# Kernel optimization log

Measured on AMD Instinct MI355X. Metric: run time of the kernel, lower is better.

## Reference

```python
import jax, jax.numpy as jnp
import numpy as np

K = 3          # deformable conv kernel size
DG = 4         # deformable groups
PAD = (K - 1) // 2


def _deform_conv(x, offset, w, dg=DG, pad=PAD):
    """DCNv1 forward (stride=1, dilation=1, conv groups=1, no bias).

    x:      [B, C, H, W]
    offset: [B, dg*K*K*2, H, W]  layout per group: (dy, dx) per kernel tap
    w:      [O, C, K, K]
    """
    B, C, H, W = x.shape
    O = w.shape[0]
    k2 = K * K
    gC = C // dg

    off = offset.reshape(B, dg, k2, 2, H, W)
    dy, dx = off[:, :, :, 0], off[:, :, :, 1]          # [B, dg, k2, H, W]

    ky, kx = jnp.meshgrid(jnp.arange(K), jnp.arange(K), indexing='ij')
    ky = ky.reshape(k2).astype(x.dtype)
    kx = kx.reshape(k2).astype(x.dtype)
    hi = jnp.arange(H, dtype=x.dtype)
    wi = jnp.arange(W, dtype=x.dtype)

    # absolute fractional sample coords: p0 - pad + kernel tap + learned offset
    ys = hi[None, None, None, :, None] - pad + ky[None, None, :, None, None] + dy
    xs = wi[None, None, None, None, :] - pad + kx[None, None, :, None, None] + dx

    y0 = jnp.floor(ys)
    x0 = jnp.floor(xs)
    ly = ys - y0   # bilinear weights
    lx = xs - x0
    y0 = y0.astype(jnp.int32)
    x0 = x0.astype(jnp.int32)

    xg = x.reshape(B, dg, gC, H * W)

    def gather(yi, xi):
        # zero padding outside the image (per-corner validity, matches mmcv)
        valid = ((yi >= 0) & (yi < H) & (xi >= 0) & (xi < W)).astype(x.dtype)
        idx = (jnp.clip(yi, 0, H - 1) * W + jnp.clip(xi, 0, W - 1)).reshape(B, dg, -1)
        vals = jax.vmap(jax.vmap(lambda t, i: t[:, i]))(xg, idx)  # [B,dg,gC,k2*H*W]
        return vals.reshape(B, dg, gC, k2, H, W) * valid[:, :, None]

    # bilinear interpolation of the 4 corners
    sampled = ((1 - ly) * (1 - lx))[:, :, None] * gather(y0,     x0) \
            + ((1 - ly) * lx      )[:, :, None] * gather(y0,     x0 + 1) \
            + (ly       * (1 - lx))[:, :, None] * gather(y0 + 1, x0) \
            + (ly       * lx      )[:, :, None] * gather(y0 + 1, x0 + 1)
    # sampled: [B, dg, gC, k2, H, W]

    wr = w.reshape(O, dg, gC, k2)
    return jnp.einsum('bgckhw,ogck->bohw', sampled, wr)


def setup_inputs() -> dict:
    key = jax.random.key(0)
    k0, k1, k2k, k3 = jax.random.split(key, 4)
    B, C, H, W, O = 2, 256, 128, 128, 256
    oc = DG * K * K * 2
    x = jax.random.normal(k0, (B, C, H, W), jnp.float32)
    # offset conv is zero-init in the module; use small random values so the
    # deformable sampling path is actually exercised
    w_offset = jax.random.normal(k1, (oc, C, 1, 1), jnp.float32) * 0.01
    b_offset = jax.random.normal(k2k, (oc,), jnp.float32) * 0.01
    w_deform = jax.random.normal(k3, (O, C, K, K), jnp.float32) / np.sqrt(C * K * K)
    return {"x": x, "w_offset": w_offset, "b_offset": b_offset, "w_deform": w_deform}


def reference(x, w_offset, b_offset, w_deform):
    # 1x1 conv predicting offsets
    offset = jnp.einsum('bchw,oc->bohw', x, w_offset[:, :, 0, 0]) \
             + b_offset[None, :, None, None]
    # deformable conv + ReLU
    return jax.nn.relu(_deform_conv(x, offset, w_deform))
```

## Files before the change

### kernel.cpp

```cpp
#include <hip/hip_runtime.h>

#define HW 16384

typedef __attribute__((ext_vector_type(4))) float f32x4;
typedef __attribute__((ext_vector_type(8))) short bf16x8;
typedef __attribute__((ext_vector_type(4))) int i32x4;

static __device__ __forceinline__ float bf2f(short s) {
    return __uint_as_float(((unsigned)(unsigned short)s) << 16);
}
static __device__ __forceinline__ unsigned short f2bf(float f) {
    unsigned u = __float_as_uint(f);
    unsigned r = u + 0x7fffu + ((u >> 16) & 1u);
    return (unsigned short)(r >> 16);
}
static __device__ __forceinline__ int cvt_pk_bf16(float lo, float hi) {
    int r;
    asm("v_cvt_pk_bf16_f32 %0, %1, %2" : "=v"(r) : "v"(lo), "v"(hi));
    return r;
}

__global__ __launch_bounds__(256) void prep_kernel(
    const float* __restrict__ x, const float* __restrict__ wd,
    const float* __restrict__ woff,
    unsigned short* __restrict__ xT, unsigned short* __restrict__ Wc2,
    unsigned short* __restrict__ Wo2)
{
    int bid = blockIdx.x;
    int tid = threadIdx.x;
    if (bid < 2048) {
        __shared__ float tl[64][65];
        int ct = bid & 3, pt = (bid >> 2) & 255, b = bid >> 10;
        int l = tid & 63, ci4 = tid >> 6;
        const float* xb = x + ((size_t)(b * 256 + ct * 64)) * HW + pt * 64;
        for (int ci = ci4; ci < 64; ci += 4)
            tl[ci][l] = xb[(size_t)ci * HW + l];
        __syncthreads();
        unsigned short* ob = xT + ((size_t)(b * HW + pt * 64)) * 256 + ct * 64;
        #pragma unroll
        for (int j2 = 0; j2 < 2; ++j2) {
            int slot = tid + j2 * 256;
            int p = slot >> 3, sl = slot & 7;
            i32x4 st;
            #pragma unroll
            for (int kq = 0; kq < 4; ++kq)
                ((int*)&st)[kq] = cvt_pk_bf16(tl[sl*8 + kq*2][p], tl[sl*8 + kq*2 + 1][p]);
            *(i32x4*)(ob + (size_t)p * 256 + sl * 8) = st;
        }
    } else if (bid < 2336) {
        int slot = (bid - 2048) * 256 + tid;
        int l  = slot & 63;
        int ks = (slot >> 6) & 1;
        int mi = (slot >> 7) & 3;
        int q  = (slot >> 9) & 3;
        int kc = slot >> 11;
        int g = kc / 9, tap = kc - g * 9;
        int o = q * 64 + mi * 16 + (l & 15);
        int cgb = (ks * 4 + (l >> 4)) * 8;
        unsigned short* dst = Wc2 + (size_t)slot * 8;
        const float* src = wd + (size_t)o * 2304 + tap;
        #pragma unroll
        for (int e = 0; e < 8; ++e)
            dst[e] = f2bf(src[(size_t)(g * 64 + cgb + e) * 9]);
    } else {
        int slot = (bid - 2336) * 256 + tid;
        int kk = slot / 320;
        int rem = slot - kk * 320;
        int o = rem >> 2, jq = rem & 3;
        unsigned short* dst = Wo2 + (size_t)slot * 8;
        #pragma unroll
        for (int e = 0; e < 8; ++e)
            dst[e] = (o < 72) ? f2bf(woff[(size_t)o * 256 + kk * 32 + jq * 8 + e]) : (unsigned short)0;
    }
}

__global__ __launch_bounds__(256, 3) void deform_kernel(
    const unsigned short* __restrict__ xT, const unsigned short* __restrict__ Wc2,
    const unsigned short* __restrict__ Wo2, const float* __restrict__ b_off,
    float* __restrict__ out)
{
    __shared__ int   c_yx[2304];
    __shared__ float c_ly[2304];
    __shared__ float c_lx[2304];
    __shared__ __align__(16) short Sl[4096];

    const int t    = threadIdx.x;
    const int lane = t & 63;
    const int q    = t >> 6;
    const int lr   = lane & 15, lq = lane >> 4;
    const int gp0  = blockIdx.x << 6;
    const int b    = gp0 >> 14;
    const int hw0  = gp0 & 16383;
    const int h    = hw0 >> 7;
    const int w0   = hw0 & 127;

    {
        bf16x8 xb[8];
        const unsigned short* xrow = xT + ((size_t)(b * HW + hw0 + q * 16 + lr)) * 256 + lq * 8;
        #pragma unroll
        for (int kk = 0; kk < 8; ++kk)
            xb[kk] = *(const bf16x8*)(xrow + kk * 32);
        #pragma unroll
        for (int mi = 0; mi < 5; ++mi) {
            f32x4 oa = (f32x4)0.f;
            #pragma unroll
            for (int kk = 0; kk < 8; ++kk) {
                bf16x8 af = *(const bf16x8*)(Wo2 + (size_t)((kk * 80 + mi * 16 + lr) * 32 + lq * 8));
                oa = __builtin_amdgcn_mfma_f32_16x16x32_bf16(af, xb[kk], oa, 0, 0, 0);
            }
            #pragma unroll
            for (int ri = 0; ri < 2; ++ri) {
                int gt = mi * 8 + lq * 2 + ri;
                if (gt < 36) {
                    int p = q * 16 + lr;
                    float dy = oa[ri * 2]     + b_off[2 * gt];
                    float dx = oa[ri * 2 + 1] + b_off[2 * gt + 1];
                    int tap = gt % 9;
                    float ys = (float)(h - 1 + tap / 3) + dy;
                    float xs = (float)(w0 + p - 1 + tap % 3) + dx;
                    float fy = floorf(ys), fx = floorf(xs);
                    int y0 = (int)fy, x0 = (int)fx;
                    c_yx[gt * 64 + p] = (y0 & 0xffff) | (x0 << 16);
                    c_ly[gt * 64 + p] = ys - fy;
                    c_lx[gt * 64 + p] = xs - fx;
                }
            }
        }
    }
    __syncthreads();

    f32x4 acc[4][4];
    #pragma unroll
    for (int mi = 0; mi < 4; ++mi)
        #pragma unroll
        for (int nj = 0; nj < 4; ++nj)
            acc[mi][nj] = (f32x4)0.f;

    const unsigned short* xbase = xT + ((size_t)b * HW) * 256;

    for (int g = 0; g < 4; ++g)
    for (int tap = 0; tap < 9; ++tap) {
        const int kc = g * 9 + tap;
        bf16x8 a_[4][2];
        {
            const unsigned short* wb = Wc2 + (size_t)(kc * 16 + q * 4) * 1024 + lane * 8;
            #pragma unroll
            for (int mi = 0; mi < 4; ++mi)
                #pragma unroll
                for (int ks = 0; ks < 2; ++ks)
                    a_[mi][ks] = *(const bf16x8*)(wb + mi * 1024 + ks * 512);
        }
        #pragma unroll
        for (int pg = 0; pg < 2; ++pg) {
            int p   = q * 16 + pg * 8 + (lane >> 3);
            int sl  = lane & 7;
            int idx = kc * 64 + p;
            int yx = c_yx[idx];
            int y0 = (int)(short)(yx & 0xffff);
            int x0 = yx >> 16;
            float ly = c_ly[idx], lx = c_lx[idx];
            float omy = 1.f - ly, omx = 1.f - lx;
            float vy0 = ((unsigned)y0       < 128u) ? 1.f : 0.f;
            float vy1 = ((unsigned)(y0 + 1) < 128u) ? 1.f : 0.f;
            float vx0 = ((unsigned)x0       < 128u) ? 1.f : 0.f;
            float vx1 = ((unsigned)(x0 + 1) < 128u) ? 1.f : 0.f;
            float w00 = omy * omx * vy0 * vx0, w01 = omy * lx * vy0 * vx1;
            float w10 = ly  * omx * vy1 * vx0, w11 = ly  * lx * vy1 * vx1;
            int y0c = min(max(y0, 0), 127), y1c = min(max(y0 + 1, 0), 127);
            int x0c = min(max(x0, 0), 127), x1c = min(max(x0 + 1, 0), 127);
            const unsigned short* cb = xbase + (size_t)(g * 64 + sl * 8);
            bf16x8 v00 = *(const bf16x8*)(cb + (size_t)(y0c * 128 + x0c) * 256);
            bf16x8 v01 = *(const bf16x8*)(cb + (size_t)(y0c * 128 + x1c) * 256);
            bf16x8 v10 = *(const bf16x8*)(cb + (size_t)(y1c * 128 + x0c) * 256);
            bf16x8 v11 = *(const bf16x8*)(cb + (size_t)(y1c * 128 + x1c) * 256);
            float sv[8];
            #pragma unroll
            for (int e = 0; e < 8; ++e)
                sv[e] = w00 * bf2f(v00[e]) + w01 * bf2f(v01[e])
                      + w10 * bf2f(v10[e]) + w11 * bf2f(v11[e]);
            i32x4 st;
            #pragma unroll
            for (int kq = 0; kq < 4; ++kq)
                ((int*)&st)[kq] = cvt_pk_bf16(sv[kq * 2], sv[kq * 2 + 1]);
            ((i32x4*)Sl)[p * 8 + (sl ^ (p & 7))] = st;
        }
        __syncthreads();
        #pragma unroll
        for (int ks = 0; ks < 2; ++ks) {
            bf16x8 bb[4];
            #pragma unroll
            for (int nj = 0; nj < 4; ++nj) {
                int pp = nj * 16 + lr;
                bb[nj] = *(const bf16x8*)&((const i32x4*)Sl)[pp * 8 + ((ks * 4 + lq) ^ (pp & 7))];
            }
            #pragma unroll
            for (int mi = 0; mi < 4; ++mi)
                #pragma unroll
                for (int nj = 0; nj < 4; ++nj)
                    acc[mi][nj] = __builtin_amdgcn_mfma_f32_16x16x32_bf16(
                        a_[mi][ks], bb[nj], acc[mi][nj], 0, 0, 0);
        }
        __syncthreads();
    }

    #pragma unroll
    for (int mi = 0; mi < 4; ++mi)
        #pragma unroll
        for (int nj = 0; nj < 4; ++nj)
            #pragma unroll
            for (int r = 0; r < 4; ++r) {
                int o  = q * 64 + mi * 16 + lq * 4 + r;
                int pp = nj * 16 + lr;
                out[((size_t)(b * 256 + o) << 14) + hw0 + pp] = fmaxf(acc[mi][nj][r], 0.f);
            }
}

extern "C" void kernel_launch(void* const* d_in, const int* in_sizes, int n_in,
                              void* d_out, int out_size, void* d_ws, size_t ws_size,
                              hipStream_t stream) {
    const float* x     = (const float*)d_in[0];
    const float* w_off = (const float*)d_in[1];
    const float* b_off = (const float*)d_in[2];
    const float* w_def = (const float*)d_in[3];
    float* out = (float*)d_out;

    unsigned short* xT  = (unsigned short*)d_ws;
    unsigned short* Wc2 = (unsigned short*)((char*)d_ws + 16777216);
    unsigned short* Wo2 = (unsigned short*)((char*)d_ws + 17956864);

    prep_kernel<<<2346, 256, 0, stream>>>(x, w_def, w_off, xT, Wc2, Wo2);
    deform_kernel<<<512, 256, 0, stream>>>(xT, Wc2, Wo2, b_off, out);
}
```

Baseline: 169.1 us.

## Double-buffer sampled tile, widen deform kernel to 512 threads, vectorize prep loads

The deform kernel now runs 512 threads per block, each wave owning 32 output channels instead of 64. Sampled-tile LDS buffers are double-buffered so the bilinear gather for the next tap overlaps the MFMA work on the current one, which drops one barrier per iteration. Block IDs are remapped across batches and rows, and the prep transpose uses float4 global loads. The cost is more LDS per block and more per-thread register pressure under the new launch bounds, which may reduce occupancy.

```diff
diff --git a/kernel.cpp b/kernel.cpp
--- a/kernel.cpp
+++ b/kernel.cpp
@@ -31,10 +31,17 @@
     if (bid < 2048) {
         __shared__ float tl[64][65];
         int ct = bid & 3, pt = (bid >> 2) & 255, b = bid >> 10;
-        int l = tid & 63, ci4 = tid >> 6;
         const float* xb = x + ((size_t)(b * 256 + ct * 64)) * HW + pt * 64;
-        for (int ci = ci4; ci < 64; ci += 4)
-            tl[ci][l] = xb[(size_t)ci * HW + l];
+        #pragma unroll
+        for (int j = 0; j < 4; ++j) {
+            int slot = tid + j * 256;
+            int c = slot >> 4, p4 = slot & 15;
+            float4 v = *(const float4*)(xb + (size_t)c * HW + p4 * 4);
+            tl[c][p4 * 4 + 0] = v.x;
+            tl[c][p4 * 4 + 1] = v.y;
+            tl[c][p4 * 4 + 2] = v.z;
+            tl[c][p4 * 4 + 3] = v.w;
+        }
         __syncthreads();
         unsigned short* ob = xT + ((size_t)(b * HW + pt * 64)) * 256 + ct * 64;
         #pragma unroll
@@ -52,10 +59,10 @@
         int l  = slot & 63;
         int ks = (slot >> 6) & 1;
         int mi = (slot >> 7) & 3;
-        int q  = (slot >> 9) & 3;
+        int q4 = (slot >> 9) & 3;
         int kc = slot >> 11;
         int g = kc / 9, tap = kc - g * 9;
-        int o = q * 64 + mi * 16 + (l & 15);
+        int o = q4 * 64 + mi * 16 + (l & 15);
         int cgb = (ks * 4 + (l >> 4)) * 8;
         unsigned short* dst = Wc2 + (size_t)slot * 8;
         const float* src = wd + (size_t)o * 2304 + tap;
@@ -74,7 +81,7 @@
     }
 }
 
-__global__ __launch_bounds__(256, 3) void deform_kernel(
+__global__ __launch_bounds__(512, 4) void deform_kernel(
     const unsigned short* __restrict__ xT, const unsigned short* __restrict__ Wc2,
     const unsigned short* __restrict__ Wo2, const float* __restrict__ b_off,
     float* __restrict__ out)
@@ -82,45 +89,49 @@
     __shared__ int   c_yx[2304];
     __shared__ float c_ly[2304];
     __shared__ float c_lx[2304];
-    __shared__ __align__(16) short Sl[4096];
+    __shared__ __align__(16) short Sbuf[2][4096];
 
     const int t    = threadIdx.x;
     const int lane = t & 63;
     const int q    = t >> 6;
     const int lr   = lane & 15, lq = lane >> 4;
-    const int gp0  = blockIdx.x << 6;
+    int bid = blockIdx.x;
+    bid = (bid & 7) * 64 + (bid >> 3);
+    const int gp0  = bid << 6;
     const int b    = gp0 >> 14;
     const int hw0  = gp0 & 16383;
     const int h    = hw0 >> 7;
     const int w0   = hw0 & 127;
 
     {
-        bf16x8 xb[8];
-        const unsigned short* xrow = xT + ((size_t)(b * HW + hw0 + q * 16 + lr)) * 256 + lq * 8;
+        const int p16 = (q & 3) * 16;
+        bf16x8 xv[8];
+        const unsigned short* xrow = xT + ((size_t)(b * HW + hw0 + p16 + lr)) * 256 + lq * 8;
         #pragma unroll
         for (int kk = 0; kk < 8; ++kk)
-            xb[kk] = *(const bf16x8*)(xrow + kk * 32);
-        #pragma unroll
-        for (int mi = 0; mi < 5; ++mi) {
+            xv[kk] = *(const bf16x8*)(xrow + kk * 32);
+        const int mi0 = (q < 4) ? 0 : 3;
+        const int nmi = (q < 4) ? 3 : 2;
+        for (int im = 0; im < nmi; ++im) {
+            int mi = mi0 + im;
             f32x4 oa = (f32x4)0.f;
             #pragma unroll
             for (int kk = 0; kk < 8; ++kk) {
                 bf16x8 af = *(const bf16x8*)(Wo2 + (size_t)((kk * 80 + mi * 16 + lr) * 32 + lq * 8));
-                oa = __builtin_amdgcn_mfma_f32_16x16x32_bf16(af, xb[kk], oa, 0, 0, 0);
+                oa = __builtin_amdgcn_mfma_f32_16x16x32_bf16(af, xv[kk], oa, 0, 0, 0);
             }
             #pragma unroll
             for (int ri = 0; ri < 2; ++ri) {
                 int gt = mi * 8 + lq * 2 + ri;
                 if (gt < 36) {
-                    int p = q * 16 + lr;
+                    int p = p16 + lr;
                     float dy = oa[ri * 2]     + b_off[2 * gt];
                     float dx = oa[ri * 2 + 1] + b_off[2 * gt + 1];
                     int tap = gt % 9;
                     float ys = (float)(h - 1 + tap / 3) + dy;
                     float xs = (float)(w0 + p - 1 + tap % 3) + dx;
                     float fy = floorf(ys), fx = floorf(xs);
-                    int y0 = (int)fy, x0 = (int)fx;
-                    c_yx[gt * 64 + p] = (y0 & 0xffff) | (x0 << 16);
+                    c_yx[gt * 64 + p] = ((int)fy & 0xffff) | ((int)fx << 16);
                     c_ly[gt * 64 + p] = ys - fy;
                     c_lx[gt * 64 + p] = xs - fx;
                 }
@@ -129,32 +140,63 @@
     }
     __syncthreads();
 
-    f32x4 acc[4][4];
+    f32x4 acc[2][4];
     #pragma unroll
-    for (int mi = 0; mi < 4; ++mi)
+    for (int mi = 0; mi < 2; ++mi)
         #pragma unroll
         for (int nj = 0; nj < 4; ++nj)
             acc[mi][nj] = (f32x4)0.f;
 
     const unsigned short* xbase = xT + ((size_t)b * HW) * 256;
-
-    for (int g = 0; g < 4; ++g)
-    for (int tap = 0; tap < 9; ++tap) {
-        const int kc = g * 9 + tap;
-        bf16x8 a_[4][2];
-        {
-            const unsigned short* wb = Wc2 + (size_t)(kc * 16 + q * 4) * 1024 + lane * 8;
-            #pragma unroll
-            for (int mi = 0; mi < 4; ++mi)
-                #pragma unroll
-                for (int ks = 0; ks < 2; ++ks)
-                    a_[mi][ks] = *(const bf16x8*)(wb + mi * 1024 + ks * 512);
-        }
-        #pragma unroll
-        for (int pg = 0; pg < 2; ++pg) {
-            int p   = q * 16 + pg * 8 + (lane >> 3);
-            int sl  = lane & 7;
-            int idx = kc * 64 + p;
+    const int ppix = q * 8 + (lane >> 3);
+    const int sl   = lane & 7;
+    const int q4   = q >> 1;
+    const int mo   = (q & 1) * 2;
+
+    {
+        int idx = ppix;
+        int yx = c_yx[idx];
+        int y0 = (int)(short)(yx & 0xffff);
+        int x0 = yx >> 16;
+        float ly = c_ly[idx], lx = c_lx[idx];
+        float omy = 1.f - ly, omx = 1.f - lx;
+        float vy0 = ((unsigned)y0       < 128u) ? 1.f : 0.f;
+        float vy1 = ((unsigned)(y0 + 1) < 128u) ? 1.f : 0.f;
+        float vx0 = ((unsigned)x0       < 128u) ? 1.f : 0.f;
+        float vx1 = ((unsigned)(x0 + 1) < 128u) ? 1.f : 0.f;
+        float w00 = omy * omx * vy0 * vx0, w01 = omy * lx * vy0 * vx1;
+        float w10 = ly  * omx * vy1 * vx0, w11 = ly  * lx * vy1 * vx1;
+        int y0c = min(max(y0, 0), 127), y1c = min(max(y0 + 1, 0), 127);
+        int x0c = min(max(x0, 0), 127), x1c = min(max(x0 + 1, 0), 127);
+        const unsigned short* cb = xbase + (size_t)(sl * 8);
+        bf16x8 v00 = *(const bf16x8*)(cb + (size_t)(y0c * 128 + x0c) * 256);
+        bf16x8 v01 = *(const bf16x8*)(cb + (size_t)(y0c * 128 + x1c) * 256);
+        bf16x8 v10 = *(const bf16x8*)(cb + (size_t)(y1c * 128 + x0c) * 256);
+        bf16x8 v11 = *(const bf16x8*)(cb + (size_t)(y1c * 128 + x1c) * 256);
+        float sv[8];
+        #pragma unroll
+        for (int e = 0; e < 8; ++e)
+            sv[e] = w00 * bf2f(v00[e]) + w01 * bf2f(v01[e])
+                  + w10 * bf2f(v10[e]) + w11 * bf2f(v11[e]);
+        i32x4 st;
+        #pragma unroll
+        for (int kq = 0; kq < 4; ++kq)
+            ((int*)&st)[kq] = cvt_pk_bf16(sv[kq * 2], sv[kq * 2 + 1]);
+        ((i32x4*)Sbuf[0])[ppix * 8 + (sl ^ (ppix & 7))] = st;
+    }
+    __syncthreads();
+
+    short* Sc = Sbuf[0];
+    short* Sn = Sbuf[1];
+
+    for (int kc = 0; kc < 36; ++kc) {
+        bf16x8 v00, v01, v10, v11;
+        float w00, w01, w10, w11;
+        const bool pf = (kc < 35);
+        if (pf) {
+            int kn = kc + 1;
+            int g  = kn / 9;
+            int idx = kn * 64 + ppix;
             int yx = c_yx[idx];
             int y0 = (int)(short)(yx & 0xffff);
             int x0 = yx >> 16;
@@ -164,15 +206,41 @@
             float vy1 = ((unsigned)(y0 + 1) < 128u) ? 1.f : 0.f;
             float vx0 = ((unsigned)x0       < 128u) ? 1.f : 0.f;
             float vx1 = ((unsigned)(x0 + 1) < 128u) ? 1.f : 0.f;
-            float w00 = omy * omx * vy0 * vx0, w01 = omy * lx * vy0 * vx1;
-            float w10 = ly  * omx * vy1 * vx0, w11 = ly  * lx * vy1 * vx1;
+            w00 = omy * omx * vy0 * vx0; w01 = omy * lx * vy0 * vx1;
+            w10 = ly  * omx * vy1 * vx0; w11 = ly  * lx * vy1 * vx1;
             int y0c = min(max(y0, 0), 127), y1c = min(max(y0 + 1, 0), 127);
             int x0c = min(max(x0, 0), 127), x1c = min(max(x0 + 1, 0), 127);
             const unsigned short* cb = xbase + (size_t)(g * 64 + sl * 8);
-            bf16x8 v00 = *(const bf16x8*)(cb + (size_t)(y0c * 128 + x0c) * 256);
-            bf16x8 v01 = *(const bf16x8*)(cb + (size_t)(y0c * 128 + x1c) * 256);
-            bf16x8 v10 = *(const bf16x8*)(cb + (size_t)(y1c * 128 + x0c) * 256);
-            bf16x8 v11 = *(const bf16x8*)(cb + (size_t)(y1c * 128 + x1c) * 256);
+            v00 = *(const bf16x8*)(cb + (size_t)(y0c * 128 + x0c) * 256);
+            v01 = *(const bf16x8*)(cb + (size_t)(y0c * 128 + x1c) * 256);
+            v10 = *(const bf16x8*)(cb + (size_t)(y1c * 128 + x0c) * 256);
+            v11 = *(const bf16x8*)(cb + (size_t)(y1c * 128 + x1c) * 256);
+        }
+        {
+            bf16x8 a_[2][2];
+            const unsigned short* wb = Wc2 + ((size_t)kc * 2048 + q4 * 512 + mo * 128 + lane) * 8;
+            #pragma unroll
+            for (int mi = 0; mi < 2; ++mi)
+                #pragma unroll
+                for (int ks = 0; ks < 2; ++ks)
+                    a_[mi][ks] = *(const bf16x8*)(wb + (mi * 128 + ks * 64) * 8);
+            #pragma unroll
+            for (int ks = 0; ks < 2; ++ks) {
+                bf16x8 bb[4];
+                #pragma unroll
+                for (int nj = 0; nj < 4; ++nj) {
+                    int pp = nj * 16 + lr;
+                    bb[nj] = *(const bf16x8*)&((const i32x4*)Sc)[pp * 8 + ((ks * 4 + lq) ^ (pp & 7))];
+                }
+                #pragma unroll
+                for (int mi = 0; mi < 2; ++mi)
+                    #pragma unroll
+                    for (int nj = 0; nj < 4; ++nj)
+                        acc[mi][nj] = __builtin_amdgcn_mfma_f32_16x16x32_bf16(
+                            a_[mi][ks], bb[nj], acc[mi][nj], 0, 0, 0);
+            }
+        }
+        if (pf) {
             float sv[8];
             #pragma unroll
             for (int e = 0; e < 8; ++e)
@@ -182,34 +250,19 @@
             #pragma unroll
             for (int kq = 0; kq < 4; ++kq)
                 ((int*)&st)[kq] = cvt_pk_bf16(sv[kq * 2], sv[kq * 2 + 1]);
-            ((i32x4*)Sl)[p * 8 + (sl ^ (p & 7))] = st;
+            ((i32x4*)Sn)[ppix * 8 + (sl ^ (ppix & 7))] = st;
         }
         __syncthreads();
-        #pragma unroll
-        for (int ks = 0; ks < 2; ++ks) {
-            bf16x8 bb[4];
-            #pragma unroll
-            for (int nj = 0; nj < 4; ++nj) {
-                int pp = nj * 16 + lr;
-                bb[nj] = *(const bf16x8*)&((const i32x4*)Sl)[pp * 8 + ((ks * 4 + lq) ^ (pp & 7))];
-            }
-            #pragma unroll
-            for (int mi = 0; mi < 4; ++mi)
-                #pragma unroll
-                for (int nj = 0; nj < 4; ++nj)
-                    acc[mi][nj] = __builtin_amdgcn_mfma_f32_16x16x32_bf16(
-                        a_[mi][ks], bb[nj], acc[mi][nj], 0, 0, 0);
-        }
-        __syncthreads();
+        short* tmp = Sc; Sc = Sn; Sn = tmp;
     }
 
     #pragma unroll
-    for (int mi = 0; mi < 4; ++mi)
+    for (int mi = 0; mi < 2; ++mi)
         #pragma unroll
         for (int nj = 0; nj < 4; ++nj)
             #pragma unroll
             for (int r = 0; r < 4; ++r) {
-                int o  = q * 64 + mi * 16 + lq * 4 + r;
+                int o  = q * 32 + mi * 16 + lq * 4 + r;
                 int pp = nj * 16 + lr;
                 out[((size_t)(b * 256 + o) << 14) + hw0 + pp] = fmaxf(acc[mi][nj][r], 0.f);
             }
@@ -229,5 +282,5 @@
     unsigned short* Wo2 = (unsigned short*)((char*)d_ws + 17956864);
 
     prep_kernel<<<2346, 256, 0, stream>>>(x, w_def, w_off, xT, Wc2, Wo2);
-    deform_kernel<<<512, 256, 0, stream>>>(xT, Wc2, Wo2, b_off, out);
-}
+    deform_kernel<<<512, 512, 0, stream>>>(xT, Wc2, Wo2, b_off, out);
+}
```

New measurement: 162.4 us. -3.9%, faster.
